# Performance work log

Measured on AMD Instinct MI355X. Metric: run time of the kernel, lower is better.

The kernel has to match this reference:

```python
import jax, jax.numpy as jnp
import numpy as np

N_HEADS = 16
WINDOW = 256


def setup_inputs() -> dict:
    key = jax.random.key(0)
    ks = jax.random.split(key, 6)
    B, S, D = 2, 2048, 1024
    std = 0.02
    x = jax.random.normal(ks[0], (B, S, D), dtype=jnp.float32)
    wq = jax.random.normal(ks[1], (D, D), dtype=jnp.float32) * std
    wk = jax.random.normal(ks[2], (D, D), dtype=jnp.float32) * std
    wv = jax.random.normal(ks[3], (D, D), dtype=jnp.float32) * std
    wo = jax.random.normal(ks[4], (D, D), dtype=jnp.float32) * std
    bq = jnp.zeros((D,), jnp.float32)
    bk = jnp.zeros((D,), jnp.float32)
    bv = jnp.zeros((D,), jnp.float32)
    bo = jnp.zeros((D,), jnp.float32)
    return {"x": x, "wq": wq, "bq": bq, "wk": wk, "bk": bk,
            "wv": wv, "bv": bv, "wo": wo, "bo": bo}


def _sliding_window_bias(seq_len: int) -> jnp.ndarray:
    # allowed iff |i - j| <= WINDOW  ->  0.0, else -inf  (matches torch loop mask)
    i = jnp.arange(seq_len)[:, None]
    j = jnp.arange(seq_len)[None, :]
    allowed = jnp.abs(i - j) <= WINDOW
    return jnp.where(allowed, 0.0, -jnp.inf).astype(jnp.float32)


def reference(x, wq, bq, wk, bk, wv, bv, wo, bo):
    B, S, D = x.shape
    H = N_HEADS
    dh = D // H
    scale = dh ** -0.5
    # nn.Linear: y = x @ W^T + b
    q = (x @ wq.T + bq).reshape(B, S, H, dh).transpose(0, 2, 1, 3)  # [B,H,S,dh]
    k = (x @ wk.T + bk).reshape(B, S, H, dh).transpose(0, 2, 1, 3)
    v = (x @ wv.T + bv).reshape(B, S, H, dh).transpose(0, 2, 1, 3)
    scores = jnp.einsum('bhqd,bhkd->bhqk', q, k) * scale  # [B,H,S,S]
    scores = scores + _sliding_window_bias(S)[None, None]
    attn = jax.nn.softmax(scores, axis=-1)
    out = jnp.einsum('bhqk,bhkd->bhqd', attn, v)  # [B,H,S,dh]
    out = out.transpose(0, 2, 1, 3).reshape(B, S, D)
    return out @ wo.T + bo
```

## Files before the change

kernel.cpp:

```cpp
#include <hip/hip_runtime.h>
#include <stdint.h>

static constexpr int Ss = 2048;
static constexpr int Dd = 1024;
static constexpr int Hh = 16;
static constexpr int DH = 64;

typedef short bf16x8 __attribute__((ext_vector_type(8)));
typedef float f32x4 __attribute__((ext_vector_type(4)));

#define LOG2E 1.4426950408889634f

__device__ __forceinline__ uint16_t f2bf(float f) {
  uint32_t u = __builtin_bit_cast(uint32_t, f);
  u += 0x7fffu + ((u >> 16) & 1u);
  return (uint16_t)(u >> 16);
}
__device__ __forceinline__ float bf2f(uint16_t h) {
  uint32_t u = ((uint32_t)h) << 16;
  return __builtin_bit_cast(float, u);
}

template <int CTRL>
__device__ __forceinline__ float dppf(float x) {
  return __builtin_bit_cast(float,
      __builtin_amdgcn_update_dpp(0, __builtin_bit_cast(int, x), CTRL, 0xF, 0xF, true));
}
__device__ __forceinline__ float rowmax16(float v) {
  v = fmaxf(v, dppf<0x128>(v));
  v = fmaxf(v, dppf<0x124>(v));
  v = fmaxf(v, dppf<0x122>(v));
  v = fmaxf(v, dppf<0x121>(v));
  return v;
}
__device__ __forceinline__ float rowsum16(float v) {
  v += dppf<0x128>(v);
  v += dppf<0x124>(v);
  v += dppf<0x122>(v);
  v += dppf<0x121>(v);
  return v;
}
__device__ __forceinline__ float fexp2(float x) { return __builtin_amdgcn_exp2f(x); }

#define GAS(p) ((const __attribute__((address_space(1))) uint32_t*)(p))
#define LAS(p) ((__attribute__((address_space(3))) uint32_t*)(p))

__global__ void cvt_all(const float* __restrict__ x,
                        const float* __restrict__ w0, const float* __restrict__ w1,
                        const float* __restrict__ w2, const float* __restrict__ w3,
                        uint16_t* __restrict__ xb,
                        uint16_t* __restrict__ o0, uint16_t* __restrict__ o1,
                        uint16_t* __restrict__ o2, uint16_t* __restrict__ o3) {
  int bid = blockIdx.x;
  const float* in;
  uint16_t* out;
  int i;
  if (bid < 4096) {
    in = x; out = xb; i = bid * 256 + threadIdx.x;
  } else {
    int b2 = bid - 4096;
    int t = b2 >> 10;
    in = (t == 0) ? w0 : (t == 1) ? w1 : (t == 2) ? w2 : w3;
    out = (t == 0) ? o0 : (t == 1) ? o1 : (t == 2) ? o2 : o3;
    i = (b2 & 1023) * 256 + threadIdx.x;
  }
  float4 v = reinterpret_cast<const float4*>(in)[i];
  ushort4 o;
  o.x = f2bf(v.x); o.y = f2bf(v.y); o.z = f2bf(v.z); o.w = f2bf(v.w);
  reinterpret_cast<ushort4*>(out)[i] = o;
}

template <int MODE, int BN>
__global__ __launch_bounds__(256, 2) void gemm_nt(
    const uint16_t* __restrict__ A,
    const uint16_t* __restrict__ W0, const uint16_t* __restrict__ W1, const uint16_t* __restrict__ W2,
    const float* __restrict__ b0, const float* __restrict__ b1, const float* __restrict__ b2,
    void* __restrict__ O0, void* __restrict__ O1, void* __restrict__ O2,
    int M, int N, int K) {
  constexpr int NI = BN / 32;
  __shared__ __align__(16) uint8_t ldsA[128 * 128];
  __shared__ __align__(16) uint8_t ldsB[BN * 128];

  const int tid = threadIdx.x, w = tid >> 6, lane = tid & 63;
  const int q = lane & 15, g = lane >> 4;
  const int wm = w >> 1, wn = w & 1;
  const int bx = blockIdx.x, by = blockIdx.y, z = blockIdx.z;
  const uint16_t* Wp = (z == 0) ? W0 : (z == 1) ? W1 : W2;
  const float* bp = (z == 0) ? b0 : (z == 1) ? b1 : b2;
  void* Op = (z == 0) ? O0 : (z == 1) ? O1 : O2;

  f32x4 acc[4][NI] = {};

  const int nkt = K >> 6;
  for (int kt = 0; kt < nkt; ++kt) {
    const int k0 = kt << 6;
    __syncthreads();
#pragma unroll
    for (int i = 0; i < 4; ++i) {
      int Lb = w * 4096 + i * 1024 + lane * 16;
      int row = Lb >> 7, cb = Lb & 127;
      int col = (cb ^ ((row & 7) << 4)) >> 1;
      const uint16_t* srcA = A + (size_t)(bx * 128 + row) * K + k0 + col;
      __builtin_amdgcn_global_load_lds(GAS(srcA), LAS(ldsA + w * 4096 + i * 1024), 16, 0, 0);
    }
#pragma unroll
    for (int i = 0; i < BN / 32; ++i) {
      int Lb = w * (BN * 32) + i * 1024 + lane * 16;
      int row = Lb >> 7, cb = Lb & 127;
      int col = (cb ^ ((row & 7) << 4)) >> 1;
      const uint16_t* srcB = Wp + (size_t)(by * BN + row) * K + k0 + col;
      __builtin_amdgcn_global_load_lds(GAS(srcB), LAS(ldsB + w * (BN * 32) + i * 1024), 16, 0, 0);
    }
    __syncthreads();

    bf16x8 af[4][2], bfg[NI][2];
#pragma unroll
    for (int mi = 0; mi < 4; ++mi)
#pragma unroll
      for (int s = 0; s < 2; ++s) {
        int row = wm * 64 + mi * 16 + q;
        int cb = (16 * g + 64 * s) ^ ((row & 7) << 4);
        af[mi][s] = *(const bf16x8*)(ldsA + row * 128 + cb);
      }
#pragma unroll
    for (int ni = 0; ni < NI; ++ni)
#pragma unroll
      for (int s = 0; s < 2; ++s) {
        int row = wn * (BN / 2) + ni * 16 + q;
        int cb = (16 * g + 64 * s) ^ ((row & 7) << 4);
        bfg[ni][s] = *(const bf16x8*)(ldsB + row * 128 + cb);
      }
#pragma unroll
    for (int mi = 0; mi < 4; ++mi)
#pragma unroll
      for (int ni = 0; ni < NI; ++ni) {
        acc[mi][ni] = __builtin_amdgcn_mfma_f32_16x16x32_bf16(af[mi][0], bfg[ni][0], acc[mi][ni], 0, 0, 0);
        acc[mi][ni] = __builtin_amdgcn_mfma_f32_16x16x32_bf16(af[mi][1], bfg[ni][1], acc[mi][ni], 0, 0, 0);
      }
  }

  float bias[NI];
#pragma unroll
  for (int ni = 0; ni < NI; ++ni) bias[ni] = bp[by * BN + wn * (BN / 2) + ni * 16 + q];
#pragma unroll
  for (int mi = 0; mi < 4; ++mi)
#pragma unroll
    for (int ni = 0; ni < NI; ++ni)
#pragma unroll
      for (int r = 0; r < 4; ++r) {
        int m = bx * 128 + wm * 64 + mi * 16 + 4 * g + r;
        int n = by * BN + wn * (BN / 2) + ni * 16 + q;
        float v = acc[mi][ni][r] + bias[ni];
        if (MODE == 0) {
          int b = m >> 11, s = m & 2047, h = n >> 6, d = n & 63;
          ((uint16_t*)Op)[(((size_t)(b * Hh + h) * Ss + s) << 6) + d] = f2bf(v);
        } else {
          ((float*)Op)[(size_t)m * N + n] = v;
        }
      }
}

__global__ __launch_bounds__(512, 4) void attn_swa(
    const uint16_t* __restrict__ Qg, const uint16_t* __restrict__ Kg,
    const uint16_t* __restrict__ Vg, uint16_t* __restrict__ Og) {
  __shared__ __align__(16) uint8_t ldsK[2][64 * 128];
  __shared__ __align__(16) uint8_t ldsVt[2][64 * 128];
  __shared__ __align__(16) uint8_t ldsP[8][2048];

  const int tid = threadIdx.x, w = tid >> 6, lane = tid & 63;
  const int q = lane & 15, g = lane >> 4;
  const int qb = blockIdx.x, bh = blockIdx.y;
  const size_t hbase = (size_t)bh * Ss * DH;
  const uint16_t* Qp = Qg + hbase;
  const uint16_t* Kp = Kg + hbase;
  const uint16_t* Vp = Vg + hbase;
  const int q0 = qb * 128;
  const int qw = q0 + w * 16;

  bf16x8 aq[2];
#pragma unroll
  for (int s = 0; s < 2; ++s) {
    bf16x8 t = *(const bf16x8*)(Qp + (size_t)(qw + q) * DH + s * 32 + g * 8);
#pragma unroll
    for (int j = 0; j < 8; ++j) {
      float f = bf2f((uint16_t)t[j]) * 0.125f;
      t[j] = (short)f2bf(f);
    }
    aq[s] = t;
  }

  f32x4 accO[4] = {};
  float mrun[4] = {-1e30f, -1e30f, -1e30f, -1e30f};
  float lrun[4] = {0.f, 0.f, 0.f, 0.f};

  const int t0 = (q0 >= 256) ? (q0 - 256) : 0;
  const int t1 = (q0 + 384 <= Ss) ? (q0 + 384) : Ss;
  const int nt = (t1 - t0) >> 6;

  {
    int Lb = w * 1024 + lane * 16;
    int row = Lb >> 7, cb = Lb & 127;
    const uint16_t* srcK = Kp + (size_t)(t0 + row) * DH + ((cb ^ ((row & 7) << 4)) >> 1);
    __builtin_amdgcn_global_load_lds(GAS(srcK), LAS(ldsK[0] + w * 1024), 16, 0, 0);
  }
  bf16x8 v0 = *(const bf16x8*)(Vp + (size_t)(t0 + lane) * DH + w * 8);

  for (int t = 0; t < nt; ++t) {
    const int kb0 = t0 + (t << 6);
    const int cur = t & 1, nxt = cur ^ 1;

    asm volatile("s_waitcnt vmcnt(0)" ::: "memory");
    uint8_t* Vt = ldsVt[cur];
#pragma unroll
    for (int j = 0; j < 8; ++j) {
      int c = w * 8 + j;
      *(uint16_t*)(Vt + c * 128 + ((2 * lane) ^ (j << 4))) = (uint16_t)v0[j];
    }
    asm volatile("s_waitcnt lgkmcnt(0)" ::: "memory");
    __builtin_amdgcn_sched_barrier(0);
    __builtin_amdgcn_s_barrier();
    __builtin_amdgcn_sched_barrier(0);

    if (t + 1 < nt) {
      int Lb = w * 1024 + lane * 16;
      int row = Lb >> 7, cb = Lb & 127;
      const uint16_t* srcK = Kp + (size_t)(kb0 + 64 + row) * DH + ((cb ^ ((row & 7) << 4)) >> 1);
      __builtin_amdgcn_global_load_lds(GAS(srcK), LAS(ldsK[nxt] + w * 1024), 16, 0, 0);
      v0 = *(const bf16x8*)(Vp + (size_t)(kb0 + 64 + lane) * DH + w * 8);
    }

    const int dtile = kb0 - qw;
    if (dtile >= -319 && dtile <= 271) {
      const uint8_t* Kl = ldsK[cur];
      f32x4 sacc[4] = {};
#pragma unroll
      for (int kb = 0; kb < 4; ++kb) {
        int row = kb * 16 + q;
#pragma unroll
        for (int s = 0; s < 2; ++s) {
          int cb = (16 * g + 64 * s) ^ ((row & 7) << 4);
          bf16x8 bk = *(const bf16x8*)(Kl + row * 128 + cb);
          sacc[kb] = __builtin_amdgcn_mfma_f32_16x16x32_bf16(aq[s], bk, sacc[kb], 0, 0, 0);
        }
      }
      if (dtile < -192 || dtile > 192) {
#pragma unroll
        for (int kb = 0; kb < 4; ++kb) {
          int key = kb0 + kb * 16 + q;
#pragma unroll
          for (int r = 0; r < 4; ++r) {
            int qi = qw + 4 * g + r;
            int dd = qi - key;
            bool ok = (dd <= 256) && (dd >= -256);
            sacc[kb][r] = ok ? sacc[kb][r] : -1e30f;
          }
        }
      }
#pragma unroll
      for (int r = 0; r < 4; ++r) {
        float tm = fmaxf(fmaxf(sacc[0][r], sacc[1][r]), fmaxf(sacc[2][r], sacc[3][r]));
        tm = rowmax16(tm);
        float mnew = fmaxf(mrun[r], tm);
        float mL = mnew * LOG2E;
        float alpha = fexp2(__builtin_fmaf(mrun[r], LOG2E, -mL));
        mrun[r] = mnew;
        float p0 = fexp2(__builtin_fmaf(sacc[0][r], LOG2E, -mL));
        float p1 = fexp2(__builtin_fmaf(sacc[1][r], LOG2E, -mL));
        float p2 = fexp2(__builtin_fmaf(sacc[2][r], LOG2E, -mL));
        float p3 = fexp2(__builtin_fmaf(sacc[3][r], LOG2E, -mL));
        sacc[0][r] = p0; sacc[1][r] = p1; sacc[2][r] = p2; sacc[3][r] = p3;
        float rs = rowsum16((p0 + p1) + (p2 + p3));
        lrun[r] = lrun[r] * alpha + rs;
#pragma unroll
        for (int db = 0; db < 4; ++db) accO[db][r] *= alpha;
      }
      uint8_t* Pl = ldsP[w];
#pragma unroll
      for (int kb = 0; kb < 4; ++kb) {
        int col2 = (kb * 16 + q) * 2;
#pragma unroll
        for (int r = 0; r < 4; ++r) {
          int prow = 4 * g + r;
          *(uint16_t*)(Pl + prow * 128 + (col2 ^ ((prow & 7) << 4))) = f2bf(sacc[kb][r]);
        }
      }
      bf16x8 ap[2];
#pragma unroll
      for (int s = 0; s < 2; ++s) {
        int cb = (16 * g + 64 * s) ^ ((q & 7) << 4);
        ap[s] = *(const bf16x8*)(Pl + q * 128 + cb);
      }
#pragma unroll
      for (int db = 0; db < 4; ++db) {
        int vr = db * 16 + q;
#pragma unroll
        for (int s = 0; s < 2; ++s) {
          int cb = (64 * s + 16 * g) ^ ((vr & 7) << 4);
          bf16x8 bvf = *(const bf16x8*)(ldsVt[cur] + vr * 128 + cb);
          accO[db] = __builtin_amdgcn_mfma_f32_16x16x32_bf16(ap[s], bvf, accO[db], 0, 0, 0);
        }
      }
    }
  }

  const int b2 = bh >> 4, h = bh & 15;
#pragma unroll
  for (int r = 0; r < 4; ++r) {
    float inv = 1.0f / lrun[r];
    int qi = qw + 4 * g + r;
    size_t rowbase = ((size_t)(b2 * Ss + qi)) * Dd + h * DH;
#pragma unroll
    for (int db = 0; db < 4; ++db) {
      Og[rowbase + db * 16 + q] = f2bf(accO[db][r] * inv);
    }
  }
}

extern "C" void kernel_launch(void* const* d_in, const int* in_sizes, int n_in,
                              void* d_out, int out_size, void* d_ws, size_t ws_size,
                              hipStream_t stream) {
  const float* x  = (const float*)d_in[0];
  const float* wq = (const float*)d_in[1];
  const float* bq = (const float*)d_in[2];
  const float* wk = (const float*)d_in[3];
  const float* bk = (const float*)d_in[4];
  const float* wv = (const float*)d_in[5];
  const float* bv = (const float*)d_in[6];
  const float* wo = (const float*)d_in[7];
  const float* bo = (const float*)d_in[8];
  float* out = (float*)d_out;

  uint8_t* ws = (uint8_t*)d_ws;
  uint16_t* xb  = (uint16_t*)(ws + (size_t)(0u  << 20));
  uint16_t* wqb = (uint16_t*)(ws + (size_t)(8u  << 20));
  uint16_t* wkb = (uint16_t*)(ws + (size_t)(10u << 20));
  uint16_t* wvb = (uint16_t*)(ws + (size_t)(12u << 20));
  uint16_t* wob = (uint16_t*)(ws + (size_t)(14u << 20));
  uint16_t* Qb  = (uint16_t*)(ws + (size_t)(16u << 20));
  uint16_t* Kb  = (uint16_t*)(ws + (size_t)(24u << 20));
  uint16_t* Vb  = (uint16_t*)(ws + (size_t)(32u << 20));
  uint16_t* AOb = (uint16_t*)(ws + (size_t)(40u << 20));

  cvt_all<<<8192, 256, 0, stream>>>(x, wq, wk, wv, wo, xb, wqb, wkb, wvb, wob);

  gemm_nt<0, 128><<<dim3(32, 8, 3), 256, 0, stream>>>(
      xb, wqb, wkb, wvb, bq, bk, bv, (void*)Qb, (void*)Kb, (void*)Vb, 4096, 1024, 1024);

  attn_swa<<<dim3(16, 32), 512, 0, stream>>>(Qb, Kb, Vb, AOb);

  gemm_nt<1, 64><<<dim3(32, 16, 1), 256, 0, stream>>>(
      AOb, wob, wob, wob, bo, bo, bo, (void*)out, (void*)out, (void*)out, 4096, 1024, 1024);
}
```

Before: 84.23 us.

## Process 32 query rows per wave to reuse K/V LDS fragments across two sub-tiles

Each attention block now covers 256 queries, with each wave handling two 16-row query sub-tiles. K and V fragments are loaded from LDS once per key tile into registers and reused for both sub-tiles. This halves the grid and the redundant K/V tile staging per query. In exchange, register pressure is higher (launch bounds drop to 2 blocks per CU), there are only 256 blocks, and the key window per block is wider.

```diff
diff --git a/kernel.cpp b/kernel.cpp
--- a/kernel.cpp
+++ b/kernel.cpp
@@ -160,7 +160,7 @@
       }
 }
 
-__global__ __launch_bounds__(512, 4) void attn_swa(
+__global__ __launch_bounds__(512, 2) void attn_swa(
     const uint16_t* __restrict__ Qg, const uint16_t* __restrict__ Kg,
     const uint16_t* __restrict__ Vg, uint16_t* __restrict__ Og) {
   __shared__ __align__(16) uint8_t ldsK[2][64 * 128];
@@ -174,27 +174,32 @@
   const uint16_t* Qp = Qg + hbase;
   const uint16_t* Kp = Kg + hbase;
   const uint16_t* Vp = Vg + hbase;
-  const int q0 = qb * 128;
-  const int qw = q0 + w * 16;
-
-  bf16x8 aq[2];
-#pragma unroll
-  for (int s = 0; s < 2; ++s) {
-    bf16x8 t = *(const bf16x8*)(Qp + (size_t)(qw + q) * DH + s * 32 + g * 8);
-#pragma unroll
-    for (int j = 0; j < 8; ++j) {
-      float f = bf2f((uint16_t)t[j]) * 0.125f;
-      t[j] = (short)f2bf(f);
-    }
-    aq[s] = t;
-  }
-
-  f32x4 accO[4] = {};
-  float mrun[4] = {-1e30f, -1e30f, -1e30f, -1e30f};
-  float lrun[4] = {0.f, 0.f, 0.f, 0.f};
+  const int q0 = qb * 256;
+  const int qw = q0 + w * 32;
+
+  bf16x8 aq[2][2];
+#pragma unroll
+  for (int h = 0; h < 2; ++h)
+#pragma unroll
+    for (int s = 0; s < 2; ++s) {
+      bf16x8 t = *(const bf16x8*)(Qp + (size_t)(qw + 16 * h + q) * DH + s * 32 + g * 8);
+#pragma unroll
+      for (int j = 0; j < 8; ++j) {
+        float f = bf2f((uint16_t)t[j]) * 0.125f;
+        t[j] = (short)f2bf(f);
+      }
+      aq[h][s] = t;
+    }
+
+  f32x4 accO[2][4] = {};
+  float mrun[2][4], lrun[2][4];
+#pragma unroll
+  for (int h = 0; h < 2; ++h)
+#pragma unroll
+    for (int r = 0; r < 4; ++r) { mrun[h][r] = -1e30f; lrun[h][r] = 0.f; }
 
   const int t0 = (q0 >= 256) ? (q0 - 256) : 0;
-  const int t1 = (q0 + 384 <= Ss) ? (q0 + 384) : Ss;
+  const int t1 = (q0 + 512 <= Ss) ? (q0 + 512) : Ss;
   const int nt = (t1 - t0) >> 6;
 
   {
@@ -230,90 +235,99 @@
     }
 
     const int dtile = kb0 - qw;
-    if (dtile >= -319 && dtile <= 271) {
+    if (dtile >= -288 && dtile <= 256) {
       const uint8_t* Kl = ldsK[cur];
-      f32x4 sacc[4] = {};
+      bf16x8 kf[4][2], vf[4][2];
 #pragma unroll
       for (int kb = 0; kb < 4; ++kb) {
         int row = kb * 16 + q;
 #pragma unroll
         for (int s = 0; s < 2; ++s) {
           int cb = (16 * g + 64 * s) ^ ((row & 7) << 4);
-          bf16x8 bk = *(const bf16x8*)(Kl + row * 128 + cb);
-          sacc[kb] = __builtin_amdgcn_mfma_f32_16x16x32_bf16(aq[s], bk, sacc[kb], 0, 0, 0);
-        }
-      }
-      if (dtile < -192 || dtile > 192) {
+          kf[kb][s] = *(const bf16x8*)(Kl + row * 128 + cb);
+          vf[kb][s] = *(const bf16x8*)(ldsVt[cur] + row * 128 + cb);
+        }
+      }
+      const bool need_mask = (dtile <= -256 || dtile >= 224);
+      uint8_t* Pl = ldsP[w];
+
+#pragma unroll
+      for (int h = 0; h < 2; ++h) {
+        const int qh = qw + 16 * h;
+        f32x4 sacc[4] = {};
 #pragma unroll
         for (int kb = 0; kb < 4; ++kb) {
-          int key = kb0 + kb * 16 + q;
+          sacc[kb] = __builtin_amdgcn_mfma_f32_16x16x32_bf16(aq[h][0], kf[kb][0], sacc[kb], 0, 0, 0);
+          sacc[kb] = __builtin_amdgcn_mfma_f32_16x16x32_bf16(aq[h][1], kf[kb][1], sacc[kb], 0, 0, 0);
+        }
+        if (need_mask) {
+#pragma unroll
+          for (int kb = 0; kb < 4; ++kb) {
+            int key = kb0 + kb * 16 + q;
+#pragma unroll
+            for (int r = 0; r < 4; ++r) {
+              int qi = qh + 4 * g + r;
+              int dd = qi - key;
+              bool ok = (dd <= 256) && (dd >= -256);
+              sacc[kb][r] = ok ? sacc[kb][r] : -1e30f;
+            }
+          }
+        }
+#pragma unroll
+        for (int r = 0; r < 4; ++r) {
+          float tm = fmaxf(fmaxf(sacc[0][r], sacc[1][r]), fmaxf(sacc[2][r], sacc[3][r]));
+          tm = rowmax16(tm);
+          float mnew = fmaxf(mrun[h][r], tm);
+          float mL = mnew * LOG2E;
+          float alpha = fexp2(__builtin_fmaf(mrun[h][r], LOG2E, -mL));
+          mrun[h][r] = mnew;
+          float p0 = fexp2(__builtin_fmaf(sacc[0][r], LOG2E, -mL));
+          float p1 = fexp2(__builtin_fmaf(sacc[1][r], LOG2E, -mL));
+          float p2 = fexp2(__builtin_fmaf(sacc[2][r], LOG2E, -mL));
+          float p3 = fexp2(__builtin_fmaf(sacc[3][r], LOG2E, -mL));
+          sacc[0][r] = p0; sacc[1][r] = p1; sacc[2][r] = p2; sacc[3][r] = p3;
+          float rs = rowsum16((p0 + p1) + (p2 + p3));
+          lrun[h][r] = lrun[h][r] * alpha + rs;
+#pragma unroll
+          for (int db = 0; db < 4; ++db) accO[h][db][r] *= alpha;
+        }
+#pragma unroll
+        for (int kb = 0; kb < 4; ++kb) {
+          int col2 = (kb * 16 + q) * 2;
 #pragma unroll
           for (int r = 0; r < 4; ++r) {
-            int qi = qw + 4 * g + r;
-            int dd = qi - key;
-            bool ok = (dd <= 256) && (dd >= -256);
-            sacc[kb][r] = ok ? sacc[kb][r] : -1e30f;
+            int prow = 4 * g + r;
+            *(uint16_t*)(Pl + prow * 128 + (col2 ^ ((prow & 7) << 4))) = f2bf(sacc[kb][r]);
           }
         }
-      }
-#pragma unroll
-      for (int r = 0; r < 4; ++r) {
-        float tm = fmaxf(fmaxf(sacc[0][r], sacc[1][r]), fmaxf(sacc[2][r], sacc[3][r]));
-        tm = rowmax16(tm);
-        float mnew = fmaxf(mrun[r], tm);
-        float mL = mnew * LOG2E;
-        float alpha = fexp2(__builtin_fmaf(mrun[r], LOG2E, -mL));
-        mrun[r] = mnew;
-        float p0 = fexp2(__builtin_fmaf(sacc[0][r], LOG2E, -mL));
-        float p1 = fexp2(__builtin_fmaf(sacc[1][r], LOG2E, -mL));
-        float p2 = fexp2(__builtin_fmaf(sacc[2][r], LOG2E, -mL));
-        float p3 = fexp2(__builtin_fmaf(sacc[3][r], LOG2E, -mL));
-        sacc[0][r] = p0; sacc[1][r] = p1; sacc[2][r] = p2; sacc[3][r] = p3;
-        float rs = rowsum16((p0 + p1) + (p2 + p3));
-        lrun[r] = lrun[r] * alpha + rs;
-#pragma unroll
-        for (int db = 0; db < 4; ++db) accO[db][r] *= alpha;
-      }
-      uint8_t* Pl = ldsP[w];
-#pragma unroll
-      for (int kb = 0; kb < 4; ++kb) {
-        int col2 = (kb * 16 + q) * 2;
-#pragma unroll
-        for (int r = 0; r < 4; ++r) {
-          int prow = 4 * g + r;
-          *(uint16_t*)(Pl + prow * 128 + (col2 ^ ((prow & 7) << 4))) = f2bf(sacc[kb][r]);
-        }
-      }
-      bf16x8 ap[2];
-#pragma unroll
-      for (int s = 0; s < 2; ++s) {
-        int cb = (16 * g + 64 * s) ^ ((q & 7) << 4);
-        ap[s] = *(const bf16x8*)(Pl + q * 128 + cb);
-      }
+        bf16x8 ap[2];
+#pragma unroll
+        for (int s = 0; s < 2; ++s) {
+          int cb = (16 * g + 64 * s) ^ ((q & 7) << 4);
+          ap[s] = *(const bf16x8*)(Pl + q * 128 + cb);
+        }
+#pragma unroll
+        for (int db = 0; db < 4; ++db) {
+          accO[h][db] = __builtin_amdgcn_mfma_f32_16x16x32_bf16(ap[0], vf[db][0], accO[h][db], 0, 0, 0);
+          accO[h][db] = __builtin_amdgcn_mfma_f32_16x16x32_bf16(ap[1], vf[db][1], accO[h][db], 0, 0, 0);
+        }
+      }
+    }
+  }
+
+  const int b2 = bh >> 4, hd = bh & 15;
+#pragma unroll
+  for (int h = 0; h < 2; ++h)
+#pragma unroll
+    for (int r = 0; r < 4; ++r) {
+      float inv = 1.0f / lrun[h][r];
+      int qi = qw + 16 * h + 4 * g + r;
+      size_t rowbase = ((size_t)(b2 * Ss + qi)) * Dd + hd * DH;
 #pragma unroll
       for (int db = 0; db < 4; ++db) {
-        int vr = db * 16 + q;
-#pragma unroll
-        for (int s = 0; s < 2; ++s) {
-          int cb = (64 * s + 16 * g) ^ ((vr & 7) << 4);
-          bf16x8 bvf = *(const bf16x8*)(ldsVt[cur] + vr * 128 + cb);
-          accO[db] = __builtin_amdgcn_mfma_f32_16x16x32_bf16(ap[s], bvf, accO[db], 0, 0, 0);
-        }
-      }
-    }
-  }
-
-  const int b2 = bh >> 4, h = bh & 15;
-#pragma unroll
-  for (int r = 0; r < 4; ++r) {
-    float inv = 1.0f / lrun[r];
-    int qi = qw + 4 * g + r;
-    size_t rowbase = ((size_t)(b2 * Ss + qi)) * Dd + h * DH;
-#pragma unroll
-    for (int db = 0; db < 4; ++db) {
-      Og[rowbase + db * 16 + q] = f2bf(accO[db][r] * inv);
-    }
-  }
+        Og[rowbase + db * 16 + q] = f2bf(accO[h][db][r] * inv);
+      }
+    }
 }
 
 extern "C" void kernel_launch(void* const* d_in, const int* in_sizes, int n_in,
@@ -346,7 +360,7 @@
   gemm_nt<0, 128><<<dim3(32, 8, 3), 256, 0, stream>>>(
       xb, wqb, wkb, wvb, bq, bk, bv, (void*)Qb, (void*)Kb, (void*)Vb, 4096, 1024, 1024);
 
-  attn_swa<<<dim3(16, 32), 512, 0, stream>>>(Qb, Kb, Vb, AOb);
+  attn_swa<<<dim3(8, 32), 512, 0, stream>>>(Qb, Kb, Vb, AOb);
 
   gemm_nt<1, 64><<<dim3(32, 16, 1), 256, 0, stream>>>(
       AOb, wob, wob, wob, bo, bo, bo, (void*)out, (void*)out, (void*)out, 4096, 1024, 1024);
```

After: 92.92 us. 10.3% more time.
